# Kernel tuning notes

Hardware: AMD Instinct MI355X
Metric: run time of the kernel (lower is better)

## Reference

```python
import jax, jax.numpy as jnp
import numpy as np

N, E, D_IN, LAT = 50000, 600000, 128, 64


def setup_inputs() -> dict:
    key = jax.random.key(0)
    ks = jax.random.split(key, 16)

    def w(k, i, o):
        return jax.random.normal(k, (i, o), jnp.float32) * (1.0 / np.sqrt(i))

    dims = [(D_IN, 64), (64, 128), (128, LAT)]
    inp = {
        "x": jax.random.normal(ks[0], (N, D_IN), jnp.float32),
        "edge_index": jax.random.randint(ks[1], (2, E), 0, N),
        "eps": jax.random.normal(ks[2], (N, LAT), jnp.float32),
    }
    for b_i, branch in enumerate(["mu", "ls"]):
        for li, (i, o) in enumerate(dims):
            inp[f"w_{branch}{li+1}"] = w(ks[3 + b_i * 3 + li], i, o)
            inp[f"b_{branch}{li+1}"] = jnp.zeros((o,), jnp.float32)
    return inp


def gcn(x, src, dst, dis, W, b):
    # GCNConv with add_self_loops=True and symmetric normalization:
    # out = D^-1/2 (A + I) D^-1/2 (x W) + b
    h = x @ W
    norm = dis[src] * dis[dst]                       # [E]
    agg = jax.ops.segment_sum(h[src] * norm[:, None], dst, num_segments=N)
    agg = agg + h * (dis * dis)[:, None]             # self-loop term d_i^-1 * h_i
    return agg + b


def encode_branch(x, src, dst, dis, ws, bs):
    h = x
    for W, b in zip(ws, bs):
        h = jax.nn.relu(gcn(h, src, dst, dis, W, b))  # ReLU after every GCNConv
    return h


def reference(x, edge_index, eps,
              w_mu1, b_mu1, w_mu2, b_mu2, w_mu3, b_mu3,
              w_ls1, b_ls1, w_ls2, b_ls2, w_ls3, b_ls3):
    src, dst = edge_index[0], edge_index[1]
    # degree with self loops (edge_weight = 1)
    deg = jax.ops.segment_sum(jnp.ones(E, x.dtype), dst, num_segments=N) + 1.0
    dis = jax.lax.rsqrt(deg)
    mu = encode_branch(x, src, dst, dis, [w_mu1, w_mu2, w_mu3], [b_mu1, b_mu2, b_mu3])
    logstd = encode_branch(x, src, dst, dis, [w_ls1, w_ls2, w_ls3], [b_ls1, b_ls2, b_ls3])
    logstd = jnp.minimum(logstd, 10.0)               # PyG VGAE MAX_LOGSTD clamp
    z = mu + eps * jnp.exp(logstd)                   # reparametrize (training=True)
    # VGAE inner-product decoder on observed edges, sigmoid=True
    adj = jax.nn.sigmoid(jnp.sum(z[src] * z[dst], axis=-1))
    return adj, mu, logstd
```

## Files before the change

### kernel.cpp

```cpp
#include <hip/hip_runtime.h>
#include <hip/hip_bf16.h>
#include <hip/hip_fp16.h>
#include <math.h>


__global__ void zero_int_k(int* __restrict__ p, int n) {
    int i = blockIdx.x * blockDim.x + threadIdx.x;
    if (i < n) p[i] = 0;
}

__global__ void count_dst_k(const int* __restrict__ ei, int* __restrict__ cnt, int E) {
    int e = blockIdx.x * blockDim.x + threadIdx.x;
    if (e < E) atomicAdd(&cnt[ei[E + e]], 1);
}

__global__ void compute_dis_k(const int* __restrict__ cnt, float* __restrict__ dis, int n) {
    int i = blockIdx.x * blockDim.x + threadIdx.x;
    if (i < n) dis[i] = rsqrtf((float)cnt[i] + 1.0f);
}

__global__ void scan1_k(const int* __restrict__ cnt, int* __restrict__ row_ptr,
                        int* __restrict__ bsum, int n) {
    __shared__ int wsum[16];
    int tid = threadIdx.x, lane = tid & 63, wv = tid >> 6;
    int i = blockIdx.x * 1024 + tid;
    int v = (i < n) ? cnt[i] : 0;
    int x = v;
#pragma unroll
    for (int off = 1; off < 64; off <<= 1) {
        int t = __shfl_up(x, off, 64);
        if (lane >= off) x += t;
    }
    if (lane == 63) wsum[wv] = x;
    __syncthreads();
    if (wv == 0 && lane < 16) {
        int y = wsum[lane];
#pragma unroll
        for (int off = 1; off < 16; off <<= 1) {
            int t = __shfl_up(y, off, 64);
            if (lane >= off) y += t;
        }
        wsum[lane] = y;
    }
    __syncthreads();
    int incl = x + ((wv == 0) ? 0 : wsum[wv - 1]);
    if (i < n) row_ptr[i + 1] = incl;
    if (tid == 1023) bsum[blockIdx.x] = incl;
}

__global__ void scan2_k(int* __restrict__ bsum, int nb) {
    int lane = threadIdx.x;
    int v = (lane < nb) ? bsum[lane] : 0;
    int x = v;
#pragma unroll
    for (int off = 1; off < 64; off <<= 1) {
        int t = __shfl_up(x, off, 64);
        if (lane >= off) x += t;
    }
    if (lane < nb) bsum[lane] = x - v;
}

__global__ void scan3_k(const int* __restrict__ cnt, int* __restrict__ row_ptr,
                        const int* __restrict__ bsum, int* __restrict__ woff, int n) {
    int i = blockIdx.x * 1024 + threadIdx.x;
    if (i == 0) row_ptr[0] = 0;
    if (i < n) {
        int r = row_ptr[i + 1] + bsum[blockIdx.x];
        row_ptr[i + 1] = r;
        woff[i] = r - cnt[i];
    }
}

__global__ void scatter_edges_k(const int* __restrict__ ei, int* __restrict__ woff,
                                int* __restrict__ src_sorted, int E) {
    int e = blockIdx.x * blockDim.x + threadIdx.x;
    if (e < E) {
        int s = ei[e];
        int d = ei[E + e];
        int pos = atomicAdd(&woff[d], 1);
        src_sorted[pos] = s;
    }
}

template <int K, int OUT, int EPI, int PRE, int AH>
__global__ __launch_bounds__(256, 4) void matmul2_k(
        const void* __restrict__ AAv, const void* __restrict__ ABv, int lda,
        int offaA, int offaB,
        const float* __restrict__ WA, const float* __restrict__ WB,
        const float* __restrict__ bA, const float* __restrict__ bB,
        __half* __restrict__ HHA, __half* __restrict__ HHB,
        const float* __restrict__ dis,
        int ldh, int offhA, int offhB, int n) {
    constexpr int TX = OUT / 4;
    constexpr int TY = 256 / TX;
    constexpr int TM = TY * 4;
    constexpr int KC = 32, KC4 = 8, KC8 = 4;
    __shared__ float w_lds[K * OUT];
    __shared__ float a_lds[TM * KC];

    int by = blockIdx.y;
    const float*  Af = (const float*)(by ? ABv : AAv);
    const __half* Ah = (const __half*)(by ? ABv : AAv);
    const float* W  = by ? WB : WA;
    const float* bi = by ? bB : bA;
    __half*      HH = by ? HHB : HHA;
    int offa = by ? offaB : offaA;
    int offh = by ? offhB : offhA;

    int tid = threadIdx.x;
    for (int idx = tid; idx < K * OUT / 4; idx += 256)
        ((float4*)w_lds)[idx] = ((const float4*)W)[idx];

    int row0 = blockIdx.x * TM;
    int tx = tid % TX;
    int ty = tid / TX;

    float4 acc[4];
#pragma unroll
    for (int i = 0; i < 4; ++i) acc[i] = make_float4(0.f, 0.f, 0.f, 0.f);

    int abase[4], akey[4];
#pragma unroll
    for (int i = 0; i < 4; ++i) {
        int r = ty * 4 + i;
        abase[i] = r * KC;
        akey[i]  = (r >> 2) & 7;
    }

    for (int kc = 0; kc < K; kc += KC) {
        __syncthreads();
        if constexpr (AH) {
            for (int f8 = tid; f8 < TM * KC8; f8 += 256) {
                int row  = f8 / KC8;
                int col8 = f8 % KC8;
                float f[8] = {0.f, 0.f, 0.f, 0.f, 0.f, 0.f, 0.f, 0.f};
                if (row0 + row < n) {
                    uint4 u = *(const uint4*)&Ah[(size_t)(row0 + row) * lda + offa + kc + col8 * 8];
                    const __half2* p = (const __half2*)&u;
#pragma unroll
                    for (int i = 0; i < 4; ++i) {
                        float2 t = __half22float2(p[i]);
                        f[2 * i] = t.x; f[2 * i + 1] = t.y;
                    }
                }
                int key = (row >> 2) & 7;
                *(float4*)&a_lds[row * KC + (((2 * col8) ^ key) << 2)] =
                    make_float4(f[0], f[1], f[2], f[3]);
                *(float4*)&a_lds[row * KC + (((2 * col8 + 1) ^ key) << 2)] =
                    make_float4(f[4], f[5], f[6], f[7]);
            }
        } else {
            for (int f4 = tid; f4 < TM * KC4; f4 += 256) {
                int row  = f4 >> 3;
                int col4 = f4 & 7;
                float4 v = make_float4(0.f, 0.f, 0.f, 0.f);
                if (row0 + row < n)
                    v = *(const float4*)&Af[(size_t)(row0 + row) * lda + offa + kc + (col4 << 2)];
                *(float4*)&a_lds[row * KC + ((col4 ^ ((row >> 2) & 7)) << 2)] = v;
            }
        }
        __syncthreads();

#pragma unroll
        for (int k = 0; k < KC; k += 4) {
            int k4 = k >> 2;
            float af[4][4];
#pragma unroll
            for (int i = 0; i < 4; ++i) {
                float4 a = *(const float4*)&a_lds[abase[i] + ((k4 ^ akey[i]) << 2)];
                af[i][0] = a.x; af[i][1] = a.y; af[i][2] = a.z; af[i][3] = a.w;
            }
#pragma unroll
            for (int j = 0; j < 4; ++j) {
                float4 wv = ((const float4*)w_lds)[(kc + k + j) * TX + tx];
#pragma unroll
                for (int i = 0; i < 4; ++i) {
                    acc[i].x += af[i][j] * wv.x;
                    acc[i].y += af[i][j] * wv.y;
                    acc[i].z += af[i][j] * wv.z;
                    acc[i].w += af[i][j] * wv.w;
                }
            }
        }
    }

#pragma unroll
    for (int i = 0; i < 4; ++i) {
        int r = row0 + ty * 4 + i;
        if (r < n) {
            float4 o = acc[i];
            if (EPI == 1) {
                float4 b = ((const float4*)bi)[tx];
                o.x = fmaxf(o.x + b.x, 0.f);
                o.y = fmaxf(o.y + b.y, 0.f);
                o.z = fmaxf(o.z + b.z, 0.f);
                o.w = fmaxf(o.w + b.w, 0.f);
            }
            float dsc = (PRE == 1) ? dis[r] : 1.f;
            __half2 h0 = __floats2half2_rn(o.x * dsc, o.y * dsc);
            __half2 h1 = __floats2half2_rn(o.z * dsc, o.w * dsc);
            uint2 u = make_uint2(*(unsigned*)&h0, *(unsigned*)&h1);
            *(uint2*)&HH[(size_t)r * ldh + offh + tx * 4] = u;
        }
    }
}

template <int MODE>
__global__ void agg2h_k(const __half* __restrict__ h, const float* __restrict__ dis,
                        const int* __restrict__ row_ptr, const int* __restrict__ srcs,
                        const float* __restrict__ bM, const float* __restrict__ bL,
                        const float* __restrict__ eps,
                        __half* __restrict__ oH,
                        float* __restrict__ oM, float* __restrict__ oL,
                        __half* __restrict__ zh, int n) {
    int wid  = (int)((blockIdx.x * (size_t)blockDim.x + threadIdx.x) >> 6);
    int lane = threadIdx.x & 63;
    if (wid >= n) return;
    int g = lane >> 4;
    int q = lane & 15;
    const __half* hq = h + 8 * q;

    __half2 acc2[4];
    if (g == 0) {
        uint4 r = *(const uint4*)&hq[(size_t)wid << 7];
        const __half2* hp = (const __half2*)&r;
#pragma unroll
        for (int i = 0; i < 4; ++i) acc2[i] = hp[i];
    } else {
        __half2 z2 = __float2half2_rn(0.f);
#pragma unroll
        for (int i = 0; i < 4; ++i) acc2[i] = z2;
    }

    int beg = row_ptr[wid], end = row_ptr[wid + 1];
    for (int cb = beg; cb < end; cb += 64) {
        int m = end - cb;
        if (m > 64) m = 64;
        int sv = 0;
        if (lane < m) sv = srcs[cb + lane];
        int j = 0;
        for (; j + 16 <= m; j += 16) {
            int s0 = __shfl(sv, j + g, 64);
            int s1 = __shfl(sv, j + 4 + g, 64);
            int s2 = __shfl(sv, j + 8 + g, 64);
            int s3 = __shfl(sv, j + 12 + g, 64);
            uint4 r0 = *(const uint4*)&hq[(size_t)s0 << 7];
            uint4 r1 = *(const uint4*)&hq[(size_t)s1 << 7];
            uint4 r2 = *(const uint4*)&hq[(size_t)s2 << 7];
            uint4 r3 = *(const uint4*)&hq[(size_t)s3 << 7];
            const __half2* p0 = (const __half2*)&r0;
            const __half2* p1 = (const __half2*)&r1;
            const __half2* p2 = (const __half2*)&r2;
            const __half2* p3 = (const __half2*)&r3;
#pragma unroll
            for (int i = 0; i < 4; ++i)
                acc2[i] = __hadd2(acc2[i],
                          __hadd2(__hadd2(p0[i], p1[i]), __hadd2(p2[i], p3[i])));
        }
        for (; j + 8 <= m; j += 8) {
            int s0 = __shfl(sv, j + g, 64);
            int s1 = __shfl(sv, j + 4 + g, 64);
            uint4 r0 = *(const uint4*)&hq[(size_t)s0 << 7];
            uint4 r1 = *(const uint4*)&hq[(size_t)s1 << 7];
            const __half2* p0 = (const __half2*)&r0;
            const __half2* p1 = (const __half2*)&r1;
#pragma unroll
            for (int i = 0; i < 4; ++i)
                acc2[i] = __hadd2(acc2[i], __hadd2(p0[i], p1[i]));
        }
        for (; j < m; j += 4) {
            int idx = j + g;
            int s0 = __shfl(sv, (idx < m) ? idx : j, 64);
            if (idx < m) {
                uint4 r0 = *(const uint4*)&hq[(size_t)s0 << 7];
                const __half2* p0 = (const __half2*)&r0;
#pragma unroll
                for (int i = 0; i < 4; ++i) acc2[i] = __hadd2(acc2[i], p0[i]);
            }
        }
    }

#pragma unroll
    for (int i = 0; i < 4; ++i) {
        int u0 = *reinterpret_cast<int*>(&acc2[i]);
        int v0 = __shfl_xor(u0, 16, 64);
        acc2[i] = __hadd2(acc2[i], *reinterpret_cast<__half2*>(&v0));
        int u1 = *reinterpret_cast<int*>(&acc2[i]);
        int v1 = __shfl_xor(u1, 32, 64);
        acc2[i] = __hadd2(acc2[i], *reinterpret_cast<__half2*>(&v1));
    }

    float di = dis[wid];
    float acc[8];
#pragma unroll
    for (int i = 0; i < 4; ++i) {
        float2 f = __half22float2(acc2[i]);
        acc[2 * i]     = f.x * di;
        acc[2 * i + 1] = f.y * di;
    }

    if (MODE == 0) {
        if (g == 0) {
            __half2 hh[4];
#pragma unroll
            for (int i = 0; i < 4; ++i) hh[i] = __floats2half2_rn(acc[2 * i], acc[2 * i + 1]);
            *(uint4*)&oH[(size_t)wid * 128 + 8 * q] = *(uint4*)hh;
        }
    } else if (MODE == 1) {
        if (g == 0) {
            const float* bs = (q < 8) ? bM + 8 * q : bL + 8 * q - 64;
            __half2 hh[4];
#pragma unroll
            for (int i = 0; i < 8; i += 2) {
                float a0 = fmaxf(acc[i] + bs[i], 0.f) * di;
                float a1 = fmaxf(acc[i + 1] + bs[i + 1], 0.f) * di;
                hh[i >> 1] = __floats2half2_rn(a0, a1);
            }
            *(uint4*)&oH[(size_t)wid * 128 + 8 * q] = *(uint4*)hh;
        }
    } else {
        const float* bs = (q < 8) ? bM + 8 * q : bL + 8 * q - 64;
        float act[8];
#pragma unroll
        for (int i = 0; i < 8; ++i) {
            float a = fmaxf(acc[i] + bs[i], 0.f);
            if (q >= 8) a = fminf(a, 10.f);
            act[i] = a;
        }
        float lsv[8];
#pragma unroll
        for (int i = 0; i < 8; ++i) lsv[i] = __shfl(act[i], lane + 8, 64);
        if (g == 0) {
            size_t ob = (size_t)wid * 64;
            if (q < 8) {
                *(float4*)&oM[ob + 8 * q]     = make_float4(act[0], act[1], act[2], act[3]);
                *(float4*)&oM[ob + 8 * q + 4] = make_float4(act[4], act[5], act[6], act[7]);
                float4 e0 = *(const float4*)&eps[ob + 8 * q];
                float4 e1 = *(const float4*)&eps[ob + 8 * q + 4];
                float zz[8];
                zz[0] = fmaf(e0.x, expf(lsv[0]), act[0]);
                zz[1] = fmaf(e0.y, expf(lsv[1]), act[1]);
                zz[2] = fmaf(e0.z, expf(lsv[2]), act[2]);
                zz[3] = fmaf(e0.w, expf(lsv[3]), act[3]);
                zz[4] = fmaf(e1.x, expf(lsv[4]), act[4]);
                zz[5] = fmaf(e1.y, expf(lsv[5]), act[5]);
                zz[6] = fmaf(e1.z, expf(lsv[6]), act[6]);
                zz[7] = fmaf(e1.w, expf(lsv[7]), act[7]);
                __half2 zh4[4];
#pragma unroll
                for (int i = 0; i < 4; ++i) zh4[i] = __floats2half2_rn(zz[2 * i], zz[2 * i + 1]);
                *(uint4*)&zh[ob + 8 * q] = *(uint4*)zh4;
            } else {
                int qq = q - 8;
                *(float4*)&oL[ob + 8 * qq]     = make_float4(act[0], act[1], act[2], act[3]);
                *(float4*)&oL[ob + 8 * qq + 4] = make_float4(act[4], act[5], act[6], act[7]);
            }
        }
    }
}

__global__ void decoder_k(const int* __restrict__ ei, const __half* __restrict__ zh,
                          float* __restrict__ adj, int E) {
    int t = blockIdx.x * 256 + threadIdx.x;
    int e = t >> 4;
    int q = threadIdx.x & 15;
    if (e >= E) return;
    int s = ei[e];
    int d = ei[E + e];
    const uint2* z2 = (const uint2*)zh;
    uint2 ua = z2[(size_t)s * 16 + q];
    uint2 ub = z2[(size_t)d * 16 + q];
    const __half2* pa = (const __half2*)&ua;
    const __half2* pb = (const __half2*)&ub;
    float p = 0.f;
#pragma unroll
    for (int i = 0; i < 2; ++i) {
        float2 fa = __half22float2(pa[i]);
        float2 fb = __half22float2(pb[i]);
        p = fmaf(fa.x, fb.x, p);
        p = fmaf(fa.y, fb.y, p);
    }
    p += __shfl_xor(p, 8);
    p += __shfl_xor(p, 4);
    p += __shfl_xor(p, 2);
    p += __shfl_xor(p, 1);
    if (q == 0) adj[e] = 1.f / (1.f + expf(-p));
}

extern "C" void kernel_launch(void* const* d_in, const int* in_sizes, int n_in,
                              void* d_out, int out_size, void* d_ws, size_t ws_size,
                              hipStream_t stream) {
    const float* x   = (const float*)d_in[0];
    const int*   ei  = (const int*)d_in[1];
    const float* eps = (const float*)d_in[2];
    const float* w_mu1 = (const float*)d_in[3];
    const float* b_mu1 = (const float*)d_in[4];
    const float* w_mu2 = (const float*)d_in[5];
    const float* b_mu2 = (const float*)d_in[6];
    const float* w_mu3 = (const float*)d_in[7];
    const float* b_mu3 = (const float*)d_in[8];
    const float* w_ls1 = (const float*)d_in[9];
    const float* b_ls1 = (const float*)d_in[10];
    const float* w_ls2 = (const float*)d_in[11];
    const float* b_ls2 = (const float*)d_in[12];
    const float* w_ls3 = (const float*)d_in[13];
    const float* b_ls3 = (const float*)d_in[14];

    const int N = in_sizes[0] / 128;
    const int E = in_sizes[1] / 2;
    const size_t NB = (size_t)N * 128;

    float* out = (float*)d_out;
    float* adj = out;
    float* mu  = out + E;
    float* ls  = out + E + (size_t)N * 64;

    float* ws = (float*)d_ws;
    __half* hpA  = (__half*)ws;
    __half* a2h  = (__half*)ws;
    __half* hpB  = (__half*)(ws + NB);
    __half* h2mu = (__half*)(ws + NB);
    __half* h2ls = h2mu + (size_t)N * 128;
    __half* zh   = (__half*)(ws + NB);
    float* c0 = ws + 2 * NB;
    const size_t P = 50176;
    float* dis         = c0;
    int*   cnt         = (int*)(c0 + P);
    int*   row_ptr     = (int*)(c0 + 2 * P);
    int*   woff        = (int*)(c0 + 3 * P);
    int*   bsum        = (int*)(c0 + 4 * P);
    int*   src_sorted  = (int*)(c0 + 4 * P + 256);

    const int nscan = (N + 1023) / 1024;

    zero_int_k<<<(N + 255) / 256, 256, 0, stream>>>(cnt, N);
    count_dst_k<<<(E + 255) / 256, 256, 0, stream>>>(ei, cnt, E);
    compute_dis_k<<<(N + 255) / 256, 256, 0, stream>>>(cnt, dis, N);
    scan1_k<<<nscan, 1024, 0, stream>>>(cnt, row_ptr, bsum, N);
    scan2_k<<<1, 64, 0, stream>>>(bsum, nscan);
    scan3_k<<<nscan, 1024, 0, stream>>>(cnt, row_ptr, bsum, woff, N);
    scatter_edges_k<<<(E + 255) / 256, 256, 0, stream>>>(ei, woff, src_sorted, E);

    const int aggBlocks = (int)(((size_t)N * 64 + 255) / 256);
    dim3 g64((N + 63) / 64, 2), g32((N + 31) / 32, 2);

    matmul2_k<128, 64, 0, 1, 0><<<g64, 256, 0, stream>>>(
        x, x, 128, 0, 0, w_mu1, w_ls1, nullptr, nullptr, hpA, hpA, dis, 128, 0, 64, N);
    agg2h_k<1><<<aggBlocks, 256, 0, stream>>>(hpA, dis, row_ptr, src_sorted,
                                              b_mu1, b_ls1, nullptr, hpB,
                                              nullptr, nullptr, nullptr, N);

    agg2h_k<0><<<aggBlocks, 256, 0, stream>>>(hpB, dis, row_ptr, src_sorted,
                                              nullptr, nullptr, nullptr, a2h,
                                              nullptr, nullptr, nullptr, N);
    matmul2_k<64, 128, 1, 0, 1><<<g32, 256, 0, stream>>>(
        a2h, a2h, 128, 0, 64, w_mu2, w_ls2, b_mu2, b_ls2, h2mu, h2ls, dis, 128, 0, 0, N);

    matmul2_k<128, 64, 0, 1, 1><<<g64, 256, 0, stream>>>(
        h2mu, h2ls, 128, 0, 0, w_mu3, w_ls3, nullptr, nullptr, hpA, hpA, dis, 128, 0, 64, N);
    agg2h_k<2><<<aggBlocks, 256, 0, stream>>>(hpA, dis, row_ptr, src_sorted,
                                              b_mu3, b_ls3, eps, nullptr,
                                              mu, ls, zh, N);

    decoder_k<<<(int)(((size_t)E * 16 + 255) / 256), 256, 0, stream>>>(ei, zh, adj, E);
}
```

Baseline: 272.0 us.

## Merge mu/logstd branch matmuls into single blocks with fp16 weights in LDS

Layer-1 and layer-2 matmuls now compute both the mu and logstd branches in one block, so the A tile is loaded and converted once instead of once per grid-y slice. The weights for both branches are stored as fp16 in LDS so they fit together. Layer 2 loads its whole 32x128 A tile up front, and the decoder uses a packed fp16 dot-product builtin. Converting weights to fp16 adds rounding error, and the extra register use and lower occupancy (launch bounds 3 for mm2) may offset the saved loads.

```diff
diff --git a/kernel.cpp b/kernel.cpp
--- a/kernel.cpp
+++ b/kernel.cpp
@@ -3,6 +3,11 @@
 #include <hip/hip_fp16.h>
 #include <math.h>
 
+
+typedef _Float16 hf2 __attribute__((ext_vector_type(2)));
+static __device__ __forceinline__ hf2 as_hf2(unsigned u) {
+    union { unsigned u; hf2 h; } c; c.u = u; return c.h;
+}
 
 __global__ void zero_int_k(int* __restrict__ p, int n) {
     int i = blockIdx.x * blockDim.x + threadIdx.x;
@@ -82,29 +87,207 @@
     }
 }
 
-template <int K, int OUT, int EPI, int PRE, int AH>
-__global__ __launch_bounds__(256, 4) void matmul2_k(
-        const void* __restrict__ AAv, const void* __restrict__ ABv, int lda,
-        int offaA, int offaB,
+__global__ __launch_bounds__(256, 4) void mm1_k(
+        const float* __restrict__ A, const float* __restrict__ WA,
+        const float* __restrict__ WB, __half* __restrict__ HH,
+        const float* __restrict__ dis, int n) {
+    constexpr int K = 128, OUT = 64, TX = 16, TY = 16, TM = 64, KC = 32, KC4 = 8;
+    __shared__ __half2 w_lds[2][K * OUT / 2];
+    __shared__ float a_lds[TM * KC];
+
+    int tid = threadIdx.x;
+    for (int idx = tid; idx < K * OUT; idx += 256) {
+        int b = idx >> 12, i2 = idx & 4095;
+        float2 w = ((const float2*)(b ? WB : WA))[i2];
+        w_lds[b][i2] = __floats2half2_rn(w.x, w.y);
+    }
+
+    int row0 = blockIdx.x * TM;
+    int tx = tid % TX, ty = tid / TX;
+
+    float4 acc[2][4];
+#pragma unroll
+    for (int b = 0; b < 2; ++b)
+#pragma unroll
+        for (int i = 0; i < 4; ++i) acc[b][i] = make_float4(0.f, 0.f, 0.f, 0.f);
+
+    int abase[4], akey[4];
+#pragma unroll
+    for (int i = 0; i < 4; ++i) {
+        int r = ty * 4 + i;
+        abase[i] = r * KC;
+        akey[i]  = (r >> 2) & 7;
+    }
+
+    for (int kc = 0; kc < K; kc += KC) {
+        __syncthreads();
+        for (int f4 = tid; f4 < TM * KC4; f4 += 256) {
+            int row = f4 >> 3, col4 = f4 & 7;
+            float4 v = make_float4(0.f, 0.f, 0.f, 0.f);
+            if (row0 + row < n)
+                v = *(const float4*)&A[(size_t)(row0 + row) * K + kc + (col4 << 2)];
+            *(float4*)&a_lds[row * KC + ((col4 ^ ((row >> 2) & 7)) << 2)] = v;
+        }
+        __syncthreads();
+
+#pragma unroll
+        for (int k = 0; k < KC; k += 4) {
+            int k4 = k >> 2;
+            float af[4][4];
+#pragma unroll
+            for (int i = 0; i < 4; ++i) {
+                float4 a = *(const float4*)&a_lds[abase[i] + ((k4 ^ akey[i]) << 2)];
+                af[i][0] = a.x; af[i][1] = a.y; af[i][2] = a.z; af[i][3] = a.w;
+            }
+#pragma unroll
+            for (int j = 0; j < 4; ++j) {
+                int widx = (kc + k + j) * (OUT / 2) + 2 * tx;
+#pragma unroll
+                for (int b = 0; b < 2; ++b) {
+                    float2 f0 = __half22float2(w_lds[b][widx]);
+                    float2 f1 = __half22float2(w_lds[b][widx + 1]);
+#pragma unroll
+                    for (int i = 0; i < 4; ++i) {
+                        acc[b][i].x += af[i][j] * f0.x;
+                        acc[b][i].y += af[i][j] * f0.y;
+                        acc[b][i].z += af[i][j] * f1.x;
+                        acc[b][i].w += af[i][j] * f1.y;
+                    }
+                }
+            }
+        }
+    }
+
+#pragma unroll
+    for (int i = 0; i < 4; ++i) {
+        int r = row0 + ty * 4 + i;
+        if (r < n) {
+            float dsc = dis[r];
+#pragma unroll
+            for (int b = 0; b < 2; ++b) {
+                float4 o = acc[b][i];
+                __half2 h0 = __floats2half2_rn(o.x * dsc, o.y * dsc);
+                __half2 h1 = __floats2half2_rn(o.z * dsc, o.w * dsc);
+                uint2 u = make_uint2(*(unsigned*)&h0, *(unsigned*)&h1);
+                *(uint2*)&HH[(size_t)r * 128 + b * 64 + tx * 4] = u;
+            }
+        }
+    }
+}
+
+__global__ __launch_bounds__(256, 3) void mm2_k(
+        const __half* __restrict__ A, const float* __restrict__ WA,
+        const float* __restrict__ WB, const float* __restrict__ bA,
+        const float* __restrict__ bB, __half* __restrict__ HA,
+        __half* __restrict__ HB, int n) {
+    constexpr int K = 64, OUT = 128, TX = 32, TM = 32;
+    __shared__ __half2 w_lds[2][K * OUT / 2];
+    __shared__ float a_lds[TM * 128];
+
+    int tid = threadIdx.x;
+    for (int idx = tid; idx < K * OUT; idx += 256) {
+        int b = idx >> 12, i2 = idx & 4095;
+        float2 w = ((const float2*)(b ? WB : WA))[i2];
+        w_lds[b][i2] = __floats2half2_rn(w.x, w.y);
+    }
+
+    int row0 = blockIdx.x * TM;
+    for (int it = tid; it < TM * 16; it += 256) {
+        int row = it >> 4, u8 = it & 15;
+        float f[8] = {0.f, 0.f, 0.f, 0.f, 0.f, 0.f, 0.f, 0.f};
+        if (row0 + row < n) {
+            uint4 u = *(const uint4*)&A[(size_t)(row0 + row) * 128 + u8 * 8];
+            const __half2* p = (const __half2*)&u;
+#pragma unroll
+            for (int i = 0; i < 4; ++i) {
+                float2 t = __half22float2(p[i]);
+                f[2 * i] = t.x; f[2 * i + 1] = t.y;
+            }
+        }
+        int key = row & 15;
+        *(float4*)&a_lds[row * 128 + (((2 * u8) ^ key) << 2)] =
+            make_float4(f[0], f[1], f[2], f[3]);
+        *(float4*)&a_lds[row * 128 + (((2 * u8 + 1) ^ key) << 2)] =
+            make_float4(f[4], f[5], f[6], f[7]);
+    }
+    __syncthreads();
+
+    int tx = tid % TX, ty = tid / TX;
+
+    float4 acc[2][4];
+#pragma unroll
+    for (int b = 0; b < 2; ++b)
+#pragma unroll
+        for (int i = 0; i < 4; ++i) acc[b][i] = make_float4(0.f, 0.f, 0.f, 0.f);
+
+#pragma unroll 4
+    for (int k4 = 0; k4 < K / 4; ++k4) {
+        float af[2][4][4];
+#pragma unroll
+        for (int b = 0; b < 2; ++b)
+#pragma unroll
+            for (int i = 0; i < 4; ++i) {
+                int r = ty * 4 + i, key = r & 15;
+                float4 a = *(const float4*)&a_lds[r * 128 + (((b * 16 + k4) ^ key) << 2)];
+                af[b][i][0] = a.x; af[b][i][1] = a.y;
+                af[b][i][2] = a.z; af[b][i][3] = a.w;
+            }
+#pragma unroll
+        for (int j = 0; j < 4; ++j) {
+            int widx = (4 * k4 + j) * (OUT / 2) + 2 * tx;
+#pragma unroll
+            for (int b = 0; b < 2; ++b) {
+                float2 f0 = __half22float2(w_lds[b][widx]);
+                float2 f1 = __half22float2(w_lds[b][widx + 1]);
+#pragma unroll
+                for (int i = 0; i < 4; ++i) {
+                    acc[b][i].x += af[b][i][j] * f0.x;
+                    acc[b][i].y += af[b][i][j] * f0.y;
+                    acc[b][i].z += af[b][i][j] * f1.x;
+                    acc[b][i].w += af[b][i][j] * f1.y;
+                }
+            }
+        }
+    }
+
+#pragma unroll
+    for (int i = 0; i < 4; ++i) {
+        int r = row0 + ty * 4 + i;
+        if (r < n) {
+#pragma unroll
+            for (int b = 0; b < 2; ++b) {
+                float4 bb = ((const float4*)(b ? bB : bA))[tx];
+                float4 o = acc[b][i];
+                o.x = fmaxf(o.x + bb.x, 0.f);
+                o.y = fmaxf(o.y + bb.y, 0.f);
+                o.z = fmaxf(o.z + bb.z, 0.f);
+                o.w = fmaxf(o.w + bb.w, 0.f);
+                __half2 h0 = __floats2half2_rn(o.x, o.y);
+                __half2 h1 = __floats2half2_rn(o.z, o.w);
+                uint2 u = make_uint2(*(unsigned*)&h0, *(unsigned*)&h1);
+                __half* H = b ? HB : HA;
+                *(uint2*)&H[(size_t)r * 128 + tx * 4] = u;
+            }
+        }
+    }
+}
+
+template <int K, int OUT>
+__global__ __launch_bounds__(256, 4) void mm3_k(
+        const __half* __restrict__ AAh, const __half* __restrict__ ABh, int lda,
         const float* __restrict__ WA, const float* __restrict__ WB,
-        const float* __restrict__ bA, const float* __restrict__ bB,
-        __half* __restrict__ HHA, __half* __restrict__ HHB,
-        const float* __restrict__ dis,
+        __half* __restrict__ HH, const float* __restrict__ dis,
         int ldh, int offhA, int offhB, int n) {
     constexpr int TX = OUT / 4;
     constexpr int TY = 256 / TX;
     constexpr int TM = TY * 4;
-    constexpr int KC = 32, KC4 = 8, KC8 = 4;
+    constexpr int KC = 32, KC8 = 4;
     __shared__ float w_lds[K * OUT];
     __shared__ float a_lds[TM * KC];
 
     int by = blockIdx.y;
-    const float*  Af = (const float*)(by ? ABv : AAv);
-    const __half* Ah = (const __half*)(by ? ABv : AAv);
-    const float* W  = by ? WB : WA;
-    const float* bi = by ? bB : bA;
-    __half*      HH = by ? HHB : HHA;
-    int offa = by ? offaB : offaA;
+    const __half* Ah = by ? ABh : AAh;
+    const float* W = by ? WB : WA;
     int offh = by ? offhB : offhA;
 
     int tid = threadIdx.x;
@@ -112,8 +295,7 @@
         ((float4*)w_lds)[idx] = ((const float4*)W)[idx];
 
     int row0 = blockIdx.x * TM;
-    int tx = tid % TX;
-    int ty = tid / TX;
+    int tx = tid % TX, ty = tid / TX;
 
     float4 acc[4];
 #pragma unroll
@@ -129,35 +311,23 @@
 
     for (int kc = 0; kc < K; kc += KC) {
         __syncthreads();
-        if constexpr (AH) {
-            for (int f8 = tid; f8 < TM * KC8; f8 += 256) {
-                int row  = f8 / KC8;
-                int col8 = f8 % KC8;
-                float f[8] = {0.f, 0.f, 0.f, 0.f, 0.f, 0.f, 0.f, 0.f};
-                if (row0 + row < n) {
-                    uint4 u = *(const uint4*)&Ah[(size_t)(row0 + row) * lda + offa + kc + col8 * 8];
-                    const __half2* p = (const __half2*)&u;
-#pragma unroll
-                    for (int i = 0; i < 4; ++i) {
-                        float2 t = __half22float2(p[i]);
-                        f[2 * i] = t.x; f[2 * i + 1] = t.y;
-                    }
+        for (int f8 = tid; f8 < TM * KC8; f8 += 256) {
+            int row = f8 / KC8, col8 = f8 % KC8;
+            float f[8] = {0.f, 0.f, 0.f, 0.f, 0.f, 0.f, 0.f, 0.f};
+            if (row0 + row < n) {
+                uint4 u = *(const uint4*)&Ah[(size_t)(row0 + row) * lda + kc + col8 * 8];
+                const __half2* p = (const __half2*)&u;
+#pragma unroll
+                for (int i = 0; i < 4; ++i) {
+                    float2 t = __half22float2(p[i]);
+                    f[2 * i] = t.x; f[2 * i + 1] = t.y;
                 }
-                int key = (row >> 2) & 7;
-                *(float4*)&a_lds[row * KC + (((2 * col8) ^ key) << 2)] =
-                    make_float4(f[0], f[1], f[2], f[3]);
-                *(float4*)&a_lds[row * KC + (((2 * col8 + 1) ^ key) << 2)] =
-                    make_float4(f[4], f[5], f[6], f[7]);
-            }
-        } else {
-            for (int f4 = tid; f4 < TM * KC4; f4 += 256) {
-                int row  = f4 >> 3;
-                int col4 = f4 & 7;
-                float4 v = make_float4(0.f, 0.f, 0.f, 0.f);
-                if (row0 + row < n)
-                    v = *(const float4*)&Af[(size_t)(row0 + row) * lda + offa + kc + (col4 << 2)];
-                *(float4*)&a_lds[row * KC + ((col4 ^ ((row >> 2) & 7)) << 2)] = v;
-            }
+            }
+            int key = (row >> 2) & 7;
+            *(float4*)&a_lds[row * KC + (((2 * col8) ^ key) << 2)] =
+                make_float4(f[0], f[1], f[2], f[3]);
+            *(float4*)&a_lds[row * KC + (((2 * col8 + 1) ^ key) << 2)] =
+                make_float4(f[4], f[5], f[6], f[7]);
         }
         __syncthreads();
 
@@ -188,15 +358,8 @@
     for (int i = 0; i < 4; ++i) {
         int r = row0 + ty * 4 + i;
         if (r < n) {
+            float dsc = dis[r];
             float4 o = acc[i];
-            if (EPI == 1) {
-                float4 b = ((const float4*)bi)[tx];
-                o.x = fmaxf(o.x + b.x, 0.f);
-                o.y = fmaxf(o.y + b.y, 0.f);
-                o.z = fmaxf(o.z + b.z, 0.f);
-                o.w = fmaxf(o.w + b.w, 0.f);
-            }
-            float dsc = (PRE == 1) ? dis[r] : 1.f;
             __half2 h0 = __floats2half2_rn(o.x * dsc, o.y * dsc);
             __half2 h1 = __floats2half2_rn(o.z * dsc, o.w * dsc);
             uint2 u = make_uint2(*(unsigned*)&h0, *(unsigned*)&h1);
@@ -370,16 +533,23 @@
     const uint2* z2 = (const uint2*)zh;
     uint2 ua = z2[(size_t)s * 16 + q];
     uint2 ub = z2[(size_t)d * 16 + q];
-    const __half2* pa = (const __half2*)&ua;
-    const __half2* pb = (const __half2*)&ub;
     float p = 0.f;
-#pragma unroll
-    for (int i = 0; i < 2; ++i) {
-        float2 fa = __half22float2(pa[i]);
-        float2 fb = __half22float2(pb[i]);
-        p = fmaf(fa.x, fb.x, p);
-        p = fmaf(fa.y, fb.y, p);
-    }
+#if defined(__has_builtin) && __has_builtin(__builtin_amdgcn_fdot2)
+    p = __builtin_amdgcn_fdot2(as_hf2(ua.x), as_hf2(ub.x), p, false);
+    p = __builtin_amdgcn_fdot2(as_hf2(ua.y), as_hf2(ub.y), p, false);
+#else
+    {
+        const __half2* pa = (const __half2*)&ua;
+        const __half2* pb = (const __half2*)&ub;
+#pragma unroll
+        for (int i = 0; i < 2; ++i) {
+            float2 fa = __half22float2(pa[i]);
+            float2 fb = __half22float2(pb[i]);
+            p = fmaf(fa.x, fb.x, p);
+            p = fmaf(fa.y, fb.y, p);
+        }
+    }
+#endif
     p += __shfl_xor(p, 8);
     p += __shfl_xor(p, 4);
     p += __shfl_xor(p, 2);
@@ -442,10 +612,8 @@
     scatter_edges_k<<<(E + 255) / 256, 256, 0, stream>>>(ei, woff, src_sorted, E);
 
     const int aggBlocks = (int)(((size_t)N * 64 + 255) / 256);
-    dim3 g64((N + 63) / 64, 2), g32((N + 31) / 32, 2);
-
-    matmul2_k<128, 64, 0, 1, 0><<<g64, 256, 0, stream>>>(
-        x, x, 128, 0, 0, w_mu1, w_ls1, nullptr, nullptr, hpA, hpA, dis, 128, 0, 64, N);
+
+    mm1_k<<<(N + 63) / 64, 256, 0, stream>>>(x, w_mu1, w_ls1, hpA, dis, N);
     agg2h_k<1><<<aggBlocks, 256, 0, stream>>>(hpA, dis, row_ptr, src_sorted,
                                               b_mu1, b_ls1, nullptr, hpB,
                                               nullptr, nullptr, nullptr, N);
@@ -453,11 +621,12 @@
     agg2h_k<0><<<aggBlocks, 256, 0, stream>>>(hpB, dis, row_ptr, src_sorted,
                                               nullptr, nullptr, nullptr, a2h,
                                               nullptr, nullptr, nullptr, N);
-    matmul2_k<64, 128, 1, 0, 1><<<g32, 256, 0, stream>>>(
-        a2h, a2h, 128, 0, 64, w_mu2, w_ls2, b_mu2, b_ls2, h2mu, h2ls, dis, 128, 0, 0, N);
-
-    matmul2_k<128, 64, 0, 1, 1><<<g64, 256, 0, stream>>>(
-        h2mu, h2ls, 128, 0, 0, w_mu3, w_ls3, nullptr, nullptr, hpA, hpA, dis, 128, 0, 64, N);
+    mm2_k<<<(N + 31) / 32, 256, 0, stream>>>(a2h, w_mu2, w_ls2, b_mu2, b_ls2,
+                                             h2mu, h2ls, N);
+
+    dim3 g64((N + 63) / 64, 2);
+    mm3_k<128, 64><<<g64, 256, 0, stream>>>(h2mu, h2ls, 128, w_mu3, w_ls3,
+                                            hpA, dis, 128, 0, 64, N);
     agg2h_k<2><<<aggBlocks, 256, 0, stream>>>(hpA, dis, row_ptr, src_sorted,
                                               b_mu3, b_ls3, eps, nullptr,
                                               mu, ls, zh, N);
```

New measurement: 377.5 us. 1.39x slower.
